# Performance work log

Measured on AMD Instinct MI355X. Metric: run time of the kernel, lower is better.

Reference implementation:

```python
import jax, jax.numpy as jnp
import numpy as np

SEQ, B = 128, 512
PT, EH, ZS, DH, NM, NMAX = 5, 256, 128, 512, 20, 256


def setup_inputs() -> dict:
    key = jax.random.key(0)
    ks = jax.random.split(key, 24)
    rn = lambda k, sh, sc=0.05: jax.random.normal(k, sh, dtype=jnp.float32) * sc
    return {
        "s": rn(ks[0], (SEQ, B, PT), 1.0),
        "enc_Wih_f": rn(ks[1], (4 * EH, PT)), "enc_Whh_f": rn(ks[2], (4 * EH, EH)), "enc_b_f": rn(ks[3], (4 * EH,)),
        "enc_Wih_b": rn(ks[4], (4 * EH, PT)), "enc_Whh_b": rn(ks[5], (4 * EH, EH)), "enc_b_b": rn(ks[6], (4 * EH,)),
        "Wmu": rn(ks[7], (ZS, 2 * EH)), "bmu": rn(ks[8], (ZS,)),
        "Wsig": rn(ks[9], (ZS, 2 * EH)), "bsig": rn(ks[10], (ZS,)),
        "Wh0": rn(ks[11], (DH, ZS)), "bh0": rn(ks[12], (DH,)),
        "dec_Wih": rn(ks[13], (4 * DH, PT + ZS)), "dec_Whh": rn(ks[14], (4 * DH, DH)), "dec_b": rn(ks[15], (4 * DH,)),
        "Wdec": rn(ks[16], (6 * NM + 3, DH)), "bdec": rn(ks[17], (6 * NM + 3,)),
        "z_eps": rn(ks[18], (B, ZS), 1.0),
        "gmm_eps": rn(ks[19], (NMAX, B, NM, 2), 1.0),
        "pen_u": jax.random.uniform(ks[20], (NMAX, B, 3), dtype=jnp.float32),
    }


def _lstm_dir(x, Wih, Whh, b, reverse):
    # PyTorch gate order: i, f, g, o. Returns final hidden state [B, H].
    H = Whh.shape[1]
    Bn = x.shape[1]
    def step(carry, xt):
        h, c = carry
        g = xt @ Wih.T + h @ Whh.T + b
        i, f, gg, o = jnp.split(g, 4, axis=-1)
        c = jax.nn.sigmoid(f) * c + jax.nn.sigmoid(i) * jnp.tanh(gg)
        h = jax.nn.sigmoid(o) * jnp.tanh(c)
        return (h, c), None
    init = (jnp.zeros((Bn, H), x.dtype), jnp.zeros((Bn, H), x.dtype))
    (h, _), _ = jax.lax.scan(step, init, x, reverse=reverse)
    return h


def reference(s, enc_Wih_f, enc_Whh_f, enc_b_f, enc_Wih_b, enc_Whh_b, enc_b_b,
              Wmu, bmu, Wsig, bsig, Wh0, bh0,
              dec_Wih, dec_Whh, dec_b, Wdec, bdec,
              z_eps, gmm_eps, pen_u):
    Bn = s.shape[1]
    # Bidirectional encoder -> concat last hidden states [B, 2*EH]
    hf = _lstm_dir(s, enc_Wih_f, enc_Whh_f, enc_b_f, False)
    hb = _lstm_dir(s, enc_Wih_b, enc_Whh_b, enc_b_b, True)
    h = jnp.concatenate([hf, hb], axis=-1)
    # Reparameterized latent
    mu = h @ Wmu.T + bmu
    sigma = jnp.exp((h @ Wsig.T + bsig) * 0.5)
    z = mu + sigma * z_eps                      # [B, ZS]
    h0 = jnp.tanh(z @ Wh0.T + bh0)              # [B, DH]
    c0 = jnp.zeros_like(h0)
    s0 = jnp.tile(jnp.array([0.0, 0.0, 1.0, 0.0, 0.0], jnp.float32), (Bn, 1))

    def step(carry, noise):
        prev, hc, cc = carry
        eps, u = noise                          # eps [B,NM,2], u [B,3]
        x = jnp.concatenate([prev, z], axis=-1)  # [B, PT+ZS]
        g = x @ dec_Wih.T + hc @ dec_Whh.T + dec_b
        i, f, gg, o = jnp.split(g, 4, axis=-1)
        cc = jax.nn.sigmoid(f) * cc + jax.nn.sigmoid(i) * jnp.tanh(gg)
        hc = jax.nn.sigmoid(o) * jnp.tanh(cc)
        y = hc @ Wdec.T + bdec                  # [B, 6*NM+3]
        mix = y[:, :6 * NM].reshape(Bn, NM, 6)
        pi = jax.nn.softmax(mix[..., 0], axis=-1)
        mx, my = mix[..., 1], mix[..., 2]
        sx, sy = jnp.exp(mix[..., 3]), jnp.exp(mix[..., 4])
        cor = jnp.tanh(mix[..., 5])
        # Sample from N(mean, [[sx^2, cor],[cor, sy^2]]) via Cholesky (cov as in source)
        l21 = cor / sx
        l22 = jnp.sqrt(jnp.maximum(sy * sy - l21 * l21, 1e-6))
        e1, e2 = eps[..., 0], eps[..., 1]
        samp_x = mx + sx * e1
        samp_y = my + l21 * e1 + l22 * e2
        dx = jnp.sum(pi * samp_x, axis=-1)      # pi-weighted sum over mixtures (as in source)
        dy = jnp.sum(pi * samp_y, axis=-1)
        q = jax.nn.softmax(y[:, -3:], axis=-1)
        pen = (u < q).astype(jnp.float32)       # independent Bernoulli thresholds, as in source
        point = jnp.concatenate([dx[:, None], dy[:, None], pen], axis=-1)
        return (point, hc, cc), point

    _, sketch = jax.lax.scan(step, (s0, h0, c0), (gmm_eps, pen_u))
    return sketch  # [NMAX, B, 5]
```

## Files before the change

### kernel.cpp

```cpp
#include <hip/hip_runtime.h>
#include <math.h>

#define B     512
#define SEQL  128
#define PT    5
#define EH    256
#define ZS    128
#define DH    512
#define NM    20
#define NMAXT 256

__device__ __forceinline__ float sigf(float x) { return 1.0f / (1.0f + expf(-x)); }

#define FMA8(m, av, lo, hi)                                                   \
    acc[m][0]=fmaf(av,lo.x,acc[m][0]); acc[m][1]=fmaf(av,lo.y,acc[m][1]);     \
    acc[m][2]=fmaf(av,lo.z,acc[m][2]); acc[m][3]=fmaf(av,lo.w,acc[m][3]);     \
    acc[m][4]=fmaf(av,hi.x,acc[m][4]); acc[m][5]=fmaf(av,hi.y,acc[m][5]);     \
    acc[m][6]=fmaf(av,hi.z,acc[m][6]); acc[m][7]=fmaf(av,hi.w,acc[m][7]);

#define XSUM(v) v += __shfl_xor(v,1); v += __shfl_xor(v,2); v += __shfl_xor(v,4); \
                v += __shfl_xor(v,8); v += __shfl_xor(v,16); v += __shfl_xor(v,32);

__global__ void transpose_pad(const float* __restrict__ in, float* __restrict__ out,
                              int rows, int cols, int rpad, long islice, long oslice)
{
    const float* ip = in + (size_t)blockIdx.z * islice;
    float* op = out + (size_t)blockIdx.z * oslice;
    int idx = blockIdx.x * 256 + threadIdx.x;
    if (idx >= cols * rpad) return;
    int c = idx / rpad, r = idx - c * rpad;
    op[idx] = (r < rows) ? ip[(size_t)r * cols + c] : 0.0f;
}

__global__ __launch_bounds__(256, 2) void enc_step3(
    const float* __restrict__ sT,
    const float* __restrict__ WihF, const float* __restrict__ WhhF, const float* __restrict__ bF,
    const float* __restrict__ WihB, const float* __restrict__ WhhB, const float* __restrict__ bB,
    const float* __restrict__ hfin, float* __restrict__ hfout, float* __restrict__ cf,
    const float* __restrict__ hbin, float* __restrict__ hbout, float* __restrict__ cb,
    int t)
{
    __shared__ float lds[8704];

    const int tid = threadIdx.x;
    const int x   = blockIdx.x;
    const int ng  = x & 31;
    const int bg  = (x >> 5) & 7;
    const int dir = x >> 8;
    const int n0  = ng * 8;
    const int b0  = bg * 64;

    const float* Whh  = dir ? WhhB : WhhF;
    const float* Wih  = dir ? WihB : WihF;
    const float* bias = dir ? bB   : bF;
    const float* hin  = dir ? hbin : hfin;
    float* hout       = dir ? hbout: hfout;
    float* c          = dir ? cb   : cf;
    const int ts = dir ? (SEQL - 1 - t) : t;

    #pragma unroll
    for (int i = 0; i < 8; ++i) {
        const int fidx = i * 256 + tid;
        const int w  = fidx >> 9;
        const int rem = fidx & 511;
        const int r  = rem >> 4, s5 = rem & 15;
        const int g  = r >> 3, nn = r & 7;
        const float4 wv = *(const float4*)&Whh[(size_t)(g * EH + n0 + nn) * EH + w * 64 + s5 * 4];
        *(float4*)&lds[((w * 32 + r) * 16 + (s5 ^ ((r >> 2) & 7))) * 4] = wv;
    }
    __syncthreads();

    const int lane = tid & 63;
    const int wv   = tid >> 6;
    const int ri   = lane & 7;
    const int bi   = lane >> 3;
    const float* hcol = hin + b0 + bi * 8;

    float acc[4][8];
    #pragma unroll
    for (int m = 0; m < 4; ++m)
        #pragma unroll
        for (int j = 0; j < 8; ++j) acc[m][j] = 0.0f;

    #pragma unroll 4
    for (int j4 = 0; j4 < 16; ++j4) {
        float4 a[4];
        #pragma unroll
        for (int m = 0; m < 4; ++m)
            a[m] = *(const float4*)&lds[((wv * 32 + ri * 4 + m) * 16 + (j4 ^ ri)) * 4];
        float4 blo[4], bhi[4];
        #pragma unroll
        for (int jj = 0; jj < 4; ++jj) {
            const float* hp = hcol + (size_t)(wv * 64 + j4 * 4 + jj) * B;
            blo[jj] = *(const float4*)hp;
            bhi[jj] = *(const float4*)(hp + 4);
        }
        #pragma unroll
        for (int m = 0; m < 4; ++m) {
            FMA8(m, a[m].x, blo[0], bhi[0])
            FMA8(m, a[m].y, blo[1], bhi[1])
            FMA8(m, a[m].z, blo[2], bhi[2])
            FMA8(m, a[m].w, blo[3], bhi[3])
        }
    }
    __syncthreads();

    #pragma unroll
    for (int m = 0; m < 4; ++m) {
        float* pr = &lds[(wv * 32 + ri * 4 + m) * 68 + bi * 8];
        *(float4*)pr       = make_float4(acc[m][0], acc[m][1], acc[m][2], acc[m][3]);
        *(float4*)(pr + 4) = make_float4(acc[m][4], acc[m][5], acc[m][6], acc[m][7]);
    }
    __syncthreads();

    const int nn = tid & 7;
    const int c0 = (tid >> 3) * 2;
    const int bgl = b0 + c0;

    float ps[4][2];
    #pragma unroll
    for (int g = 0; g < 4; ++g) {
        const int r = g * 8 + nn;
        ps[g][0] = lds[r * 68 + c0]     + lds[(32 + r) * 68 + c0]
                 + lds[(64 + r) * 68 + c0] + lds[(96 + r) * 68 + c0];
        ps[g][1] = lds[r * 68 + c0 + 1] + lds[(32 + r) * 68 + c0 + 1]
                 + lds[(64 + r) * 68 + c0 + 1] + lds[(96 + r) * 68 + c0 + 1];
    }

    #pragma unroll
    for (int bb2 = 0; bb2 < 2; ++bb2) {
        const int b = bgl + bb2;
        float gv[4];
        const float x0 = sT[((size_t)ts * PT + 0) * B + b];
        const float x1 = sT[((size_t)ts * PT + 1) * B + b];
        const float x2 = sT[((size_t)ts * PT + 2) * B + b];
        const float x3 = sT[((size_t)ts * PT + 3) * B + b];
        const float x4 = sT[((size_t)ts * PT + 4) * B + b];
        #pragma unroll
        for (int g = 0; g < 4; ++g) {
            const int grow = g * EH + n0 + nn;
            const float* wr = Wih + (size_t)grow * PT;
            float v = ps[g][bb2] + bias[grow];
            v = fmaf(x0, wr[0], v); v = fmaf(x1, wr[1], v); v = fmaf(x2, wr[2], v);
            v = fmaf(x3, wr[3], v); v = fmaf(x4, wr[4], v);
            gv[g] = v;
        }
        const size_t idx = (size_t)(n0 + nn) * B + b;
        const float cv = sigf(gv[1]) * c[idx] + sigf(gv[0]) * tanhf(gv[2]);
        c[idx] = cv;
        hout[idx] = sigf(gv[3]) * tanhf(cv);
    }
}

__global__ __launch_bounds__(256, 2) void dec_step3(
    const float* __restrict__ hin, float* __restrict__ hout, float* __restrict__ cT,
    const float* __restrict__ CzT, const float* __restrict__ Whh,
    const float* __restrict__ Wih, const float* __restrict__ prevPt, int t)
{
    __shared__ float lds[16384];

    const int tid = threadIdx.x;
    const int x   = blockIdx.x;
    const int ng  = x & 63;
    const int bg  = x >> 6;
    const int n0  = ng * 8;
    const int b0  = bg * 64;

    #pragma unroll
    for (int i = 0; i < 16; ++i) {
        const int fidx = i * 256 + tid;
        const int w   = fidx >> 10;
        const int rem = fidx & 1023;
        const int r   = rem >> 5, s5 = rem & 31;
        const int g   = r >> 3, nn = r & 7;
        const int sl  = (s5 & 16) | ((s5 & 15) ^ ((r >> 2) & 7));
        const float4 wv = *(const float4*)&Whh[(size_t)(g * DH + n0 + nn) * DH + w * 128 + s5 * 4];
        *(float4*)&lds[((w * 32 + r) * 32 + sl) * 4] = wv;
    }
    __syncthreads();

    const int lane = tid & 63;
    const int wv   = tid >> 6;
    const int ri   = lane & 7;
    const int bi   = lane >> 3;
    const float* hcol = hin + b0 + bi * 8;

    float acc[4][8];
    #pragma unroll
    for (int m = 0; m < 4; ++m)
        #pragma unroll
        for (int j = 0; j < 8; ++j) acc[m][j] = 0.0f;

    #pragma unroll
    for (int cc = 0; cc < 2; ++cc) {
        const int kb = wv * 128 + cc * 64;
        #pragma unroll 4
        for (int j4 = 0; j4 < 16; ++j4) {
            float4 a[4];
            #pragma unroll
            for (int m = 0; m < 4; ++m)
                a[m] = *(const float4*)&lds[((wv * 32 + ri * 4 + m) * 32 + cc * 16 + (j4 ^ ri)) * 4];
            float4 blo[4], bhi[4];
            #pragma unroll
            for (int jj = 0; jj < 4; ++jj) {
                const float* hp = hcol + (size_t)(kb + j4 * 4 + jj) * B;
                blo[jj] = *(const float4*)hp;
                bhi[jj] = *(const float4*)(hp + 4);
            }
            #pragma unroll
            for (int m = 0; m < 4; ++m) {
                FMA8(m, a[m].x, blo[0], bhi[0])
                FMA8(m, a[m].y, blo[1], bhi[1])
                FMA8(m, a[m].z, blo[2], bhi[2])
                FMA8(m, a[m].w, blo[3], bhi[3])
            }
        }
    }
    __syncthreads();

    #pragma unroll
    for (int m = 0; m < 4; ++m) {
        float* pr = &lds[(wv * 32 + ri * 4 + m) * 68 + bi * 8];
        *(float4*)pr       = make_float4(acc[m][0], acc[m][1], acc[m][2], acc[m][3]);
        *(float4*)(pr + 4) = make_float4(acc[m][4], acc[m][5], acc[m][6], acc[m][7]);
    }
    __syncthreads();

    const int nn = tid & 7;
    const int c0 = (tid >> 3) * 2;
    const int bgl = b0 + c0;

    float ps[4][2];
    #pragma unroll
    for (int g = 0; g < 4; ++g) {
        const int r = g * 8 + nn;
        ps[g][0] = lds[r * 68 + c0]     + lds[(32 + r) * 68 + c0]
                 + lds[(64 + r) * 68 + c0] + lds[(96 + r) * 68 + c0];
        ps[g][1] = lds[r * 68 + c0 + 1] + lds[(32 + r) * 68 + c0 + 1]
                 + lds[(64 + r) * 68 + c0 + 1] + lds[(96 + r) * 68 + c0 + 1];
    }

    #pragma unroll
    for (int bb2 = 0; bb2 < 2; ++bb2) {
        const int b = bgl + bb2;
        float p0, p1, p2, p3, p4;
        if (t == 0) { p0 = 0.f; p1 = 0.f; p2 = 1.f; p3 = 0.f; p4 = 0.f; }
        else {
            const float* pp = &prevPt[(size_t)b * 5];
            p0 = pp[0]; p1 = pp[1]; p2 = pp[2]; p3 = pp[3]; p4 = pp[4];
        }
        float gv[4];
        #pragma unroll
        for (int g = 0; g < 4; ++g) {
            const int grow = g * DH + n0 + nn;
            const float* wr = Wih + (size_t)grow * 133;
            float v = ps[g][bb2] + CzT[(size_t)grow * B + b];
            v = fmaf(p0, wr[0], v); v = fmaf(p1, wr[1], v); v = fmaf(p2, wr[2], v);
            v = fmaf(p3, wr[3], v); v = fmaf(p4, wr[4], v);
            gv[g] = v;
        }
        const size_t idx = (size_t)(n0 + nn) * B + b;
        const float cv = sigf(gv[1]) * cT[idx] + sigf(gv[0]) * tanhf(gv[2]);
        cT[idx] = cv;
        hout[idx] = sigf(gv[3]) * tanhf(cv);
    }
}

__global__ __launch_bounds__(256) void ysamp4(
    const float* __restrict__ hT, const float* __restrict__ WdecT,
    const float* __restrict__ bdec,
    const float* __restrict__ geps, const float* __restrict__ penu,
    float* __restrict__ out, int t)
{
    __shared__ float part[2][2][128];
    __shared__ float Y[2][128];

    const int tid = threadIdx.x;
    const int col = tid & 127;
    const int ks  = tid >> 7;
    const int b0  = blockIdx.x * 2;

    float a0 = 0.f, a1 = 0.f;
    const float* wp = WdecT + (size_t)ks * 256 * 128 + col;
    const float* hp = hT + (size_t)ks * 256 * B + b0;
    #pragma unroll 8
    for (int k = 0; k < 256; ++k) {
        const float w  = wp[(size_t)k * 128];
        const float2 h2 = *(const float2*)(hp + (size_t)k * B);
        a0 = fmaf(w, h2.x, a0);
        a1 = fmaf(w, h2.y, a1);
    }
    part[ks][0][col] = a0;
    part[ks][1][col] = a1;
    __syncthreads();
    if (ks == 0) {
        const float bd = (col < 123) ? bdec[col] : 0.0f;
        Y[0][col] = part[0][0][col] + part[1][0][col] + bd;
        Y[1][col] = part[0][1][col] + part[1][1][col] + bd;
    }
    __syncthreads();

    if (tid < 128) {
        const int bp   = tid >> 6;
        const int lane = tid & 63;
        const int b    = b0 + bp;
        const float* y = Y[bp];

        const int m = lane;
        float pv = (m < NM) ? y[6 * m] : -1e30f;
        float mm = pv;
        mm = fmaxf(mm, __shfl_xor(mm, 1));  mm = fmaxf(mm, __shfl_xor(mm, 2));
        mm = fmaxf(mm, __shfl_xor(mm, 4));  mm = fmaxf(mm, __shfl_xor(mm, 8));
        mm = fmaxf(mm, __shfl_xor(mm, 16)); mm = fmaxf(mm, __shfl_xor(mm, 32));
        float pe = 0.f, tx = 0.f, ty = 0.f;
        if (m < NM) {
            pe = expf(pv - mm);
            const float mx = y[6 * m + 1], my = y[6 * m + 2];
            const float sx = expf(y[6 * m + 3]), sy = expf(y[6 * m + 4]);
            const float cor = tanhf(y[6 * m + 5]);
            const float l21 = cor / sx;
            const float l22 = sqrtf(fmaxf(sy * sy - l21 * l21, 1e-6f));
            const float* ep = &geps[(((size_t)t * B) + b) * (NM * 2) + 2 * m];
            const float e1 = ep[0], e2 = ep[1];
            tx = pe * fmaf(sx, e1, mx);
            ty = pe * (my + fmaf(l21, e1, l22 * e2));
        }
        XSUM(pe) XSUM(tx) XSUM(ty)
        if (lane == 0) {
            const float q0 = y[120], q1 = y[121], q2 = y[122];
            const float qm = fmaxf(q0, fmaxf(q1, q2));
            const float e0 = expf(q0 - qm), e1q = expf(q1 - qm), e2q = expf(q2 - qm);
            const float qs = e0 + e1q + e2q;
            const float* u = &penu[(((size_t)t * B) + b) * 3];
            float* o = &out[(((size_t)t * B) + b) * 5];
            o[0] = tx / pe;
            o[1] = ty / pe;
            o[2] = (u[0] < e0  / qs) ? 1.f : 0.f;
            o[3] = (u[1] < e1q / qs) ? 1.f : 0.f;
            o[4] = (u[2] < e2q / qs) ? 1.f : 0.f;
        }
    }
}

__global__ __launch_bounds__(256) void latent2(
    const float* __restrict__ hfT, const float* __restrict__ hbT,
    const float* __restrict__ Wmu, const float* __restrict__ bmu,
    const float* __restrict__ Wsig, const float* __restrict__ bsig,
    const float* __restrict__ zepsT, float* __restrict__ zT)
{
    const int lane = threadIdx.x & 63;
    const int wv   = __builtin_amdgcn_readfirstlane(threadIdx.x >> 6);
    const int b    = blockIdx.x * 64 + lane;
    const int n0   = blockIdx.y * 8 + wv * 2;

    float am[2] = {}, as2[2] = {};
    #pragma unroll 4
    for (int k0 = 0; k0 < 2 * EH; k0 += 4) {
        const float* hsrc = (k0 < EH) ? hfT : hbT;
        const int kk = k0 & (EH - 1);
        const float a0 = hsrc[(size_t)(kk + 0) * B + b];
        const float a1 = hsrc[(size_t)(kk + 1) * B + b];
        const float a2 = hsrc[(size_t)(kk + 2) * B + b];
        const float a3 = hsrc[(size_t)(kk + 3) * B + b];
        #pragma unroll
        for (int j = 0; j < 2; ++j) {
            const float4 wm = *(const float4*)&Wmu[((size_t)(n0 + j)) * (2 * EH) + k0];
            const float4 ws = *(const float4*)&Wsig[((size_t)(n0 + j)) * (2 * EH) + k0];
            float u = am[j], v = as2[j];
            u = fmaf(a0, wm.x, u); u = fmaf(a1, wm.y, u); u = fmaf(a2, wm.z, u); u = fmaf(a3, wm.w, u);
            v = fmaf(a0, ws.x, v); v = fmaf(a1, ws.y, v); v = fmaf(a2, ws.z, v); v = fmaf(a3, ws.w, v);
            am[j] = u; as2[j] = v;
        }
    }
    #pragma unroll
    for (int j = 0; j < 2; ++j) {
        const int n = n0 + j;
        const float mu = am[j] + bmu[n];
        const float sg = expf(0.5f * (as2[j] + bsig[n]));
        zT[(size_t)n * B + b] = fmaf(sg, zepsT[(size_t)n * B + b], mu);
    }
}

__global__ __launch_bounds__(256) void h02(
    const float* __restrict__ zT, const float* __restrict__ Wh0,
    const float* __restrict__ bh0, float* __restrict__ hT)
{
    const int lane = threadIdx.x & 63;
    const int wv   = __builtin_amdgcn_readfirstlane(threadIdx.x >> 6);
    const int b    = blockIdx.x * 64 + lane;
    const int n0   = blockIdx.y * 32 + wv * 8;

    float acc[8] = {};
    #pragma unroll 2
    for (int k0 = 0; k0 < ZS; k0 += 4) {
        const float a0 = zT[(size_t)(k0 + 0) * B + b];
        const float a1 = zT[(size_t)(k0 + 1) * B + b];
        const float a2 = zT[(size_t)(k0 + 2) * B + b];
        const float a3 = zT[(size_t)(k0 + 3) * B + b];
        #pragma unroll
        for (int r = 0; r < 8; ++r) {
            const float4 w = *(const float4*)&Wh0[((size_t)(n0 + r)) * ZS + k0];
            float v = acc[r];
            v = fmaf(a0, w.x, v); v = fmaf(a1, w.y, v);
            v = fmaf(a2, w.z, v); v = fmaf(a3, w.w, v);
            acc[r] = v;
        }
    }
    #pragma unroll
    for (int r = 0; r < 8; ++r)
        hT[(size_t)(n0 + r) * B + b] = tanhf(acc[r] + bh0[n0 + r]);
}

__global__ __launch_bounds__(256) void cz2(
    const float* __restrict__ zT, const float* __restrict__ Wih,
    const float* __restrict__ bias, float* __restrict__ CzT)
{
    const int lane = threadIdx.x & 63;
    const int wv   = __builtin_amdgcn_readfirstlane(threadIdx.x >> 6);
    const int b    = blockIdx.x * 64 + lane;
    const int r0   = blockIdx.y * 32 + wv * 8;

    float acc[8] = {};
    #pragma unroll 4
    for (int k = 0; k < ZS; ++k) {
        const float a = zT[(size_t)k * B + b];
        #pragma unroll
        for (int r = 0; r < 8; ++r)
            acc[r] = fmaf(a, Wih[(size_t)(r0 + r) * 133 + 5 + k], acc[r]);
    }
    #pragma unroll
    for (int r = 0; r < 8; ++r)
        CzT[(size_t)(r0 + r) * B + b] = acc[r] + bias[r0 + r];
}

extern "C" void kernel_launch(void* const* d_in, const int* in_sizes, int n_in,
                              void* d_out, int out_size, void* d_ws, size_t ws_size,
                              hipStream_t stream)
{
    (void)in_sizes; (void)n_in; (void)out_size; (void)ws_size;

    const float* s      = (const float*)d_in[0];
    const float* WihF   = (const float*)d_in[1];
    const float* WhhF   = (const float*)d_in[2];
    const float* bF     = (const float*)d_in[3];
    const float* WihB   = (const float*)d_in[4];
    const float* WhhB   = (const float*)d_in[5];
    const float* bB     = (const float*)d_in[6];
    const float* Wmu    = (const float*)d_in[7];
    const float* bmu    = (const float*)d_in[8];
    const float* Wsig   = (const float*)d_in[9];
    const float* bsig   = (const float*)d_in[10];
    const float* Wh0    = (const float*)d_in[11];
    const float* bh0    = (const float*)d_in[12];
    const float* decWih = (const float*)d_in[13];
    const float* decWhh = (const float*)d_in[14];
    const float* decB   = (const float*)d_in[15];
    const float* Wdec   = (const float*)d_in[16];
    const float* bdec   = (const float*)d_in[17];
    const float* zeps   = (const float*)d_in[18];
    const float* geps   = (const float*)d_in[19];
    const float* penu   = (const float*)d_in[20];

    float* out = (float*)d_out;
    float* p   = (float*)d_ws;

    float* hf0  = p; p += 131072;
    float* hb0  = p; p += 131072;
    float* cf   = p; p += 131072;
    float* cb   = p; p += 131072;
    float* cdT  = p; p += 262144;
    float* hf1  = p; p += 131072;
    float* hb1  = p; p += 131072;
    float* hA   = p; p += 262144;
    float* hB   = p; p += 262144;
    float* zT   = p; p += 65536;
    float* CzT  = p; p += 1048576;
    float* zepsT= p; p += 65536;
    float* WdecT= p; p += 65536;
    float* sT   = p; p += 327680;

    hipMemsetAsync((void*)hf0, 0, (size_t)(4 * 131072 + 262144) * sizeof(float), stream);

    transpose_pad<<<dim3(256, 1, 1), 256, 0, stream>>>(zeps, zepsT, B, ZS, B, 0, 0);
    transpose_pad<<<dim3(256, 1, 1), 256, 0, stream>>>(Wdec, WdecT, 123, DH, 128, 0, 0);
    transpose_pad<<<dim3(10, 1, SEQL), 256, 0, stream>>>(s, sT, B, PT, B, (long)B * PT, (long)B * PT);

    for (int t = 0; t < SEQL; ++t) {
        const float* hfin = (t & 1) ? hf1 : hf0;  float* hfout = (t & 1) ? hf0 : hf1;
        const float* hbin = (t & 1) ? hb1 : hb0;  float* hbout = (t & 1) ? hb0 : hb1;
        enc_step3<<<dim3(512), 256, 0, stream>>>(
            sT, WihF, WhhF, bF, WihB, WhhB, bB,
            hfin, hfout, cf, hbin, hbout, cb, t);
    }
    latent2<<<dim3(8, 16), 256, 0, stream>>>(hf0, hb0, Wmu, bmu, Wsig, bsig, zepsT, zT);
    h02<<<dim3(8, 16), 256, 0, stream>>>(zT, Wh0, bh0, hA);
    cz2<<<dim3(8, 64), 256, 0, stream>>>(zT, decWih, decB, CzT);

    for (int t = 0; t < NMAXT; ++t) {
        const float* hin = (t & 1) ? hB : hA;
        float* hout      = (t & 1) ? hA : hB;
        dec_step3<<<dim3(512), 256, 0, stream>>>(
            hin, hout, cdT, CzT, decWhh, decWih,
            t ? (out + (size_t)(t - 1) * B * 5) : out, t);
        ysamp4<<<dim3(256), 256, 0, stream>>>(hout, WdecT, bdec, geps, penu, out, t);
    }
}
```

Baseline: 12.23 ms.

## Double threads per block and split K across 8 waves in LSTM step kernels

The encoder and decoder step kernels now launch with 512 threads, and the K reduction is split across 8 waves instead of 4, followed by an 8-way partial-sum reduction in LDS. Each thread's epilogue now handles one batch column instead of two. The output sampling kernel now uses one batch element per block with a 4-way K split over 512 blocks. The aim is more latency hiding and parallelism in these small, latency-bound recurrent steps, at the cost of larger LDS use and an extra reduction step.

```diff
diff --git a/kernel.cpp b/kernel.cpp
--- a/kernel.cpp
+++ b/kernel.cpp
@@ -32,7 +32,7 @@
     op[idx] = (r < rows) ? ip[(size_t)r * cols + c] : 0.0f;
 }
 
-__global__ __launch_bounds__(256, 2) void enc_step3(
+__global__ __launch_bounds__(512, 4) void enc_step4(
     const float* __restrict__ sT,
     const float* __restrict__ WihF, const float* __restrict__ WhhF, const float* __restrict__ bF,
     const float* __restrict__ WihB, const float* __restrict__ WhhB, const float* __restrict__ bB,
@@ -40,7 +40,7 @@
     const float* __restrict__ hbin, float* __restrict__ hbout, float* __restrict__ cb,
     int t)
 {
-    __shared__ float lds[8704];
+    __shared__ float lds[17408];
 
     const int tid = threadIdx.x;
     const int x   = blockIdx.x;
@@ -59,14 +59,14 @@
     const int ts = dir ? (SEQL - 1 - t) : t;
 
     #pragma unroll
-    for (int i = 0; i < 8; ++i) {
-        const int fidx = i * 256 + tid;
-        const int w  = fidx >> 9;
+    for (int i = 0; i < 4; ++i) {
+        const int fidx = i * 512 + tid;
+        const int w   = fidx >> 9;
         const int rem = fidx & 511;
-        const int r  = rem >> 4, s5 = rem & 15;
-        const int g  = r >> 3, nn = r & 7;
-        const float4 wv = *(const float4*)&Whh[(size_t)(g * EH + n0 + nn) * EH + w * 64 + s5 * 4];
-        *(float4*)&lds[((w * 32 + r) * 16 + (s5 ^ ((r >> 2) & 7))) * 4] = wv;
+        const int r   = rem >> 4, s5 = rem & 15;
+        const int g   = r >> 3, nn = r & 7;
+        const float4 wv4 = *(const float4*)&Whh[(size_t)(g * EH + n0 + nn) * EH + w * 64 + s5 * 4];
+        *(float4*)&lds[((w * 32 + r) * 16 + (s5 ^ ((r >> 2) & 7))) * 4] = wv4;
     }
     __syncthreads();
 
@@ -74,6 +74,8 @@
     const int wv   = tid >> 6;
     const int ri   = lane & 7;
     const int bi   = lane >> 3;
+    const int wq   = wv >> 1;
+    const int sb   = (wv & 1) * 8;
     const float* hcol = hin + b0 + bi * 8;
 
     float acc[4][8];
@@ -82,25 +84,23 @@
         #pragma unroll
         for (int j = 0; j < 8; ++j) acc[m][j] = 0.0f;
 
-    #pragma unroll 4
-    for (int j4 = 0; j4 < 16; ++j4) {
+    #pragma unroll 2
+    for (int j4 = 0; j4 < 8; ++j4) {
         float4 a[4];
         #pragma unroll
         for (int m = 0; m < 4; ++m)
-            a[m] = *(const float4*)&lds[((wv * 32 + ri * 4 + m) * 16 + (j4 ^ ri)) * 4];
-        float4 blo[4], bhi[4];
+            a[m] = *(const float4*)&lds[((wq * 32 + ri * 4 + m) * 16 + (sb | (j4 ^ ri))) * 4];
+        const int kb = wv * 32 + j4 * 4;
         #pragma unroll
         for (int jj = 0; jj < 4; ++jj) {
-            const float* hp = hcol + (size_t)(wv * 64 + j4 * 4 + jj) * B;
-            blo[jj] = *(const float4*)hp;
-            bhi[jj] = *(const float4*)(hp + 4);
-        }
-        #pragma unroll
-        for (int m = 0; m < 4; ++m) {
-            FMA8(m, a[m].x, blo[0], bhi[0])
-            FMA8(m, a[m].y, blo[1], bhi[1])
-            FMA8(m, a[m].z, blo[2], bhi[2])
-            FMA8(m, a[m].w, blo[3], bhi[3])
+            const float* hp = hcol + (size_t)(kb + jj) * B;
+            const float4 blo = *(const float4*)hp;
+            const float4 bhi = *(const float4*)(hp + 4);
+            #pragma unroll
+            for (int m = 0; m < 4; ++m) {
+                const float av = (jj == 0) ? a[m].x : (jj == 1) ? a[m].y : (jj == 2) ? a[m].z : a[m].w;
+                FMA8(m, av, blo, bhi)
+            }
         }
     }
     __syncthreads();
@@ -114,50 +114,46 @@
     __syncthreads();
 
     const int nn = tid & 7;
-    const int c0 = (tid >> 3) * 2;
-    const int bgl = b0 + c0;
-
-    float ps[4][2];
+    const int c0 = tid >> 3;
+    const int b  = b0 + c0;
+
+    float ps[4];
     #pragma unroll
     for (int g = 0; g < 4; ++g) {
         const int r = g * 8 + nn;
-        ps[g][0] = lds[r * 68 + c0]     + lds[(32 + r) * 68 + c0]
-                 + lds[(64 + r) * 68 + c0] + lds[(96 + r) * 68 + c0];
-        ps[g][1] = lds[r * 68 + c0 + 1] + lds[(32 + r) * 68 + c0 + 1]
-                 + lds[(64 + r) * 68 + c0 + 1] + lds[(96 + r) * 68 + c0 + 1];
-    }
-
-    #pragma unroll
-    for (int bb2 = 0; bb2 < 2; ++bb2) {
-        const int b = bgl + bb2;
-        float gv[4];
-        const float x0 = sT[((size_t)ts * PT + 0) * B + b];
-        const float x1 = sT[((size_t)ts * PT + 1) * B + b];
-        const float x2 = sT[((size_t)ts * PT + 2) * B + b];
-        const float x3 = sT[((size_t)ts * PT + 3) * B + b];
-        const float x4 = sT[((size_t)ts * PT + 4) * B + b];
-        #pragma unroll
-        for (int g = 0; g < 4; ++g) {
-            const int grow = g * EH + n0 + nn;
-            const float* wr = Wih + (size_t)grow * PT;
-            float v = ps[g][bb2] + bias[grow];
-            v = fmaf(x0, wr[0], v); v = fmaf(x1, wr[1], v); v = fmaf(x2, wr[2], v);
-            v = fmaf(x3, wr[3], v); v = fmaf(x4, wr[4], v);
-            gv[g] = v;
-        }
-        const size_t idx = (size_t)(n0 + nn) * B + b;
-        const float cv = sigf(gv[1]) * c[idx] + sigf(gv[0]) * tanhf(gv[2]);
-        c[idx] = cv;
-        hout[idx] = sigf(gv[3]) * tanhf(cv);
-    }
-}
-
-__global__ __launch_bounds__(256, 2) void dec_step3(
+        float v = 0.0f;
+        #pragma unroll
+        for (int w8 = 0; w8 < 8; ++w8) v += lds[(w8 * 32 + r) * 68 + c0];
+        ps[g] = v;
+    }
+
+    const float x0 = sT[((size_t)ts * PT + 0) * B + b];
+    const float x1 = sT[((size_t)ts * PT + 1) * B + b];
+    const float x2 = sT[((size_t)ts * PT + 2) * B + b];
+    const float x3 = sT[((size_t)ts * PT + 3) * B + b];
+    const float x4 = sT[((size_t)ts * PT + 4) * B + b];
+    float gv[4];
+    #pragma unroll
+    for (int g = 0; g < 4; ++g) {
+        const int grow = g * EH + n0 + nn;
+        const float* wr = Wih + (size_t)grow * PT;
+        float v = ps[g] + bias[grow];
+        v = fmaf(x0, wr[0], v); v = fmaf(x1, wr[1], v); v = fmaf(x2, wr[2], v);
+        v = fmaf(x3, wr[3], v); v = fmaf(x4, wr[4], v);
+        gv[g] = v;
+    }
+    const size_t idx = (size_t)(n0 + nn) * B + b;
+    const float cv = sigf(gv[1]) * c[idx] + sigf(gv[0]) * tanhf(gv[2]);
+    c[idx] = cv;
+    hout[idx] = sigf(gv[3]) * tanhf(cv);
+}
+
+__global__ __launch_bounds__(512, 4) void dec_step4(
     const float* __restrict__ hin, float* __restrict__ hout, float* __restrict__ cT,
     const float* __restrict__ CzT, const float* __restrict__ Whh,
     const float* __restrict__ Wih, const float* __restrict__ prevPt, int t)
 {
-    __shared__ float lds[16384];
+    __shared__ float lds[17408];
 
     const int tid = threadIdx.x;
     const int x   = blockIdx.x;
@@ -167,15 +163,15 @@
     const int b0  = bg * 64;
 
     #pragma unroll
-    for (int i = 0; i < 16; ++i) {
-        const int fidx = i * 256 + tid;
+    for (int i = 0; i < 8; ++i) {
+        const int fidx = i * 512 + tid;
         const int w   = fidx >> 10;
         const int rem = fidx & 1023;
         const int r   = rem >> 5, s5 = rem & 31;
         const int g   = r >> 3, nn = r & 7;
         const int sl  = (s5 & 16) | ((s5 & 15) ^ ((r >> 2) & 7));
-        const float4 wv = *(const float4*)&Whh[(size_t)(g * DH + n0 + nn) * DH + w * 128 + s5 * 4];
-        *(float4*)&lds[((w * 32 + r) * 32 + sl) * 4] = wv;
+        const float4 wv4 = *(const float4*)&Whh[(size_t)(g * DH + n0 + nn) * DH + w * 128 + s5 * 4];
+        *(float4*)&lds[((w * 32 + r) * 32 + sl) * 4] = wv4;
     }
     __syncthreads();
 
@@ -183,6 +179,8 @@
     const int wv   = tid >> 6;
     const int ri   = lane & 7;
     const int bi   = lane >> 3;
+    const int wq   = wv >> 1;
+    const int sb   = (wv & 1) * 16;
     const float* hcol = hin + b0 + bi * 8;
 
     float acc[4][8];
@@ -191,28 +189,22 @@
         #pragma unroll
         for (int j = 0; j < 8; ++j) acc[m][j] = 0.0f;
 
-    #pragma unroll
-    for (int cc = 0; cc < 2; ++cc) {
-        const int kb = wv * 128 + cc * 64;
-        #pragma unroll 4
-        for (int j4 = 0; j4 < 16; ++j4) {
-            float4 a[4];
-            #pragma unroll
-            for (int m = 0; m < 4; ++m)
-                a[m] = *(const float4*)&lds[((wv * 32 + ri * 4 + m) * 32 + cc * 16 + (j4 ^ ri)) * 4];
-            float4 blo[4], bhi[4];
-            #pragma unroll
-            for (int jj = 0; jj < 4; ++jj) {
-                const float* hp = hcol + (size_t)(kb + j4 * 4 + jj) * B;
-                blo[jj] = *(const float4*)hp;
-                bhi[jj] = *(const float4*)(hp + 4);
-            }
+    #pragma unroll 2
+    for (int j4 = 0; j4 < 16; ++j4) {
+        float4 a[4];
+        #pragma unroll
+        for (int m = 0; m < 4; ++m)
+            a[m] = *(const float4*)&lds[((wq * 32 + ri * 4 + m) * 32 + (sb | (j4 ^ ri))) * 4];
+        const int kb = wv * 64 + j4 * 4;
+        #pragma unroll
+        for (int jj = 0; jj < 4; ++jj) {
+            const float* hp = hcol + (size_t)(kb + jj) * B;
+            const float4 blo = *(const float4*)hp;
+            const float4 bhi = *(const float4*)(hp + 4);
             #pragma unroll
             for (int m = 0; m < 4; ++m) {
-                FMA8(m, a[m].x, blo[0], bhi[0])
-                FMA8(m, a[m].y, blo[1], bhi[1])
-                FMA8(m, a[m].z, blo[2], bhi[2])
-                FMA8(m, a[m].w, blo[3], bhi[3])
+                const float av = (jj == 0) ? a[m].x : (jj == 1) ? a[m].y : (jj == 2) ? a[m].z : a[m].w;
+                FMA8(m, av, blo, bhi)
             }
         }
     }
@@ -227,85 +219,71 @@
     __syncthreads();
 
     const int nn = tid & 7;
-    const int c0 = (tid >> 3) * 2;
-    const int bgl = b0 + c0;
-
-    float ps[4][2];
+    const int c0 = tid >> 3;
+    const int b  = b0 + c0;
+
+    float ps[4];
     #pragma unroll
     for (int g = 0; g < 4; ++g) {
         const int r = g * 8 + nn;
-        ps[g][0] = lds[r * 68 + c0]     + lds[(32 + r) * 68 + c0]
-                 + lds[(64 + r) * 68 + c0] + lds[(96 + r) * 68 + c0];
-        ps[g][1] = lds[r * 68 + c0 + 1] + lds[(32 + r) * 68 + c0 + 1]
-                 + lds[(64 + r) * 68 + c0 + 1] + lds[(96 + r) * 68 + c0 + 1];
-    }
-
-    #pragma unroll
-    for (int bb2 = 0; bb2 < 2; ++bb2) {
-        const int b = bgl + bb2;
-        float p0, p1, p2, p3, p4;
-        if (t == 0) { p0 = 0.f; p1 = 0.f; p2 = 1.f; p3 = 0.f; p4 = 0.f; }
-        else {
-            const float* pp = &prevPt[(size_t)b * 5];
-            p0 = pp[0]; p1 = pp[1]; p2 = pp[2]; p3 = pp[3]; p4 = pp[4];
-        }
-        float gv[4];
-        #pragma unroll
-        for (int g = 0; g < 4; ++g) {
-            const int grow = g * DH + n0 + nn;
-            const float* wr = Wih + (size_t)grow * 133;
-            float v = ps[g][bb2] + CzT[(size_t)grow * B + b];
-            v = fmaf(p0, wr[0], v); v = fmaf(p1, wr[1], v); v = fmaf(p2, wr[2], v);
-            v = fmaf(p3, wr[3], v); v = fmaf(p4, wr[4], v);
-            gv[g] = v;
-        }
-        const size_t idx = (size_t)(n0 + nn) * B + b;
-        const float cv = sigf(gv[1]) * cT[idx] + sigf(gv[0]) * tanhf(gv[2]);
-        cT[idx] = cv;
-        hout[idx] = sigf(gv[3]) * tanhf(cv);
-    }
-}
-
-__global__ __launch_bounds__(256) void ysamp4(
+        float v = 0.0f;
+        #pragma unroll
+        for (int w8 = 0; w8 < 8; ++w8) v += lds[(w8 * 32 + r) * 68 + c0];
+        ps[g] = v;
+    }
+
+    float p0, p1, p2, p3, p4;
+    if (t == 0) { p0 = 0.f; p1 = 0.f; p2 = 1.f; p3 = 0.f; p4 = 0.f; }
+    else {
+        const float* pp = &prevPt[(size_t)b * 5];
+        p0 = pp[0]; p1 = pp[1]; p2 = pp[2]; p3 = pp[3]; p4 = pp[4];
+    }
+    float gv[4];
+    #pragma unroll
+    for (int g = 0; g < 4; ++g) {
+        const int grow = g * DH + n0 + nn;
+        const float* wr = Wih + (size_t)grow * 133;
+        float v = ps[g] + CzT[(size_t)grow * B + b];
+        v = fmaf(p0, wr[0], v); v = fmaf(p1, wr[1], v); v = fmaf(p2, wr[2], v);
+        v = fmaf(p3, wr[3], v); v = fmaf(p4, wr[4], v);
+        gv[g] = v;
+    }
+    const size_t idx = (size_t)(n0 + nn) * B + b;
+    const float cv = sigf(gv[1]) * cT[idx] + sigf(gv[0]) * tanhf(gv[2]);
+    cT[idx] = cv;
+    hout[idx] = sigf(gv[3]) * tanhf(cv);
+}
+
+__global__ __launch_bounds__(512) void ysamp5(
     const float* __restrict__ hT, const float* __restrict__ WdecT,
     const float* __restrict__ bdec,
     const float* __restrict__ geps, const float* __restrict__ penu,
     float* __restrict__ out, int t)
 {
-    __shared__ float part[2][2][128];
-    __shared__ float Y[2][128];
+    __shared__ float part[4][128];
+    __shared__ float Y[128];
 
     const int tid = threadIdx.x;
     const int col = tid & 127;
     const int ks  = tid >> 7;
-    const int b0  = blockIdx.x * 2;
-
-    float a0 = 0.f, a1 = 0.f;
-    const float* wp = WdecT + (size_t)ks * 256 * 128 + col;
-    const float* hp = hT + (size_t)ks * 256 * B + b0;
+    const int b   = blockIdx.x;
+
+    float a0 = 0.f;
+    const float* wp = WdecT + (size_t)ks * 128 * 128 + col;
+    const float* hp = hT + (size_t)ks * 128 * B + b;
     #pragma unroll 8
-    for (int k = 0; k < 256; ++k) {
-        const float w  = wp[(size_t)k * 128];
-        const float2 h2 = *(const float2*)(hp + (size_t)k * B);
-        a0 = fmaf(w, h2.x, a0);
-        a1 = fmaf(w, h2.y, a1);
-    }
-    part[ks][0][col] = a0;
-    part[ks][1][col] = a1;
-    __syncthreads();
-    if (ks == 0) {
-        const float bd = (col < 123) ? bdec[col] : 0.0f;
-        Y[0][col] = part[0][0][col] + part[1][0][col] + bd;
-        Y[1][col] = part[0][1][col] + part[1][1][col] + bd;
-    }
-    __syncthreads();
-
-    if (tid < 128) {
-        const int bp   = tid >> 6;
-        const int lane = tid & 63;
-        const int b    = b0 + bp;
-        const float* y = Y[bp];
-
+    for (int k = 0; k < 128; ++k)
+        a0 = fmaf(wp[(size_t)k * 128], hp[(size_t)k * B], a0);
+    part[ks][col] = a0;
+    __syncthreads();
+    if (ks == 0)
+        Y[col] = part[0][col] + part[1][col] + part[2][col] + part[3][col]
+               + ((col < 123) ? bdec[col] : 0.0f);
+    __syncthreads();
+
+    if (tid < 64) {
+        const int lane = tid;
+        const float* y = Y;
         const int m = lane;
         float pv = (m < NM) ? y[6 * m] : -1e30f;
         float mm = pv;
@@ -488,7 +466,7 @@
     for (int t = 0; t < SEQL; ++t) {
         const float* hfin = (t & 1) ? hf1 : hf0;  float* hfout = (t & 1) ? hf0 : hf1;
         const float* hbin = (t & 1) ? hb1 : hb0;  float* hbout = (t & 1) ? hb0 : hb1;
-        enc_step3<<<dim3(512), 256, 0, stream>>>(
+        enc_step4<<<dim3(512), 512, 0, stream>>>(
             sT, WihF, WhhF, bF, WihB, WhhB, bB,
             hfin, hfout, cf, hbin, hbout, cb, t);
     }
@@ -499,9 +477,9 @@
     for (int t = 0; t < NMAXT; ++t) {
         const float* hin = (t & 1) ? hB : hA;
         float* hout      = (t & 1) ? hA : hB;
-        dec_step3<<<dim3(512), 256, 0, stream>>>(
+        dec_step4<<<dim3(512), 512, 0, stream>>>(
             hin, hout, cdT, CzT, decWhh, decWih,
             t ? (out + (size_t)(t - 1) * B * 5) : out, t);
-        ysamp4<<<dim3(256), 256, 0, stream>>>(hout, WdecT, bdec, geps, penu, out, t);
-    }
-}
+        ysamp5<<<dim3(512), 512, 0, stream>>>(hout, WdecT, bdec, geps, penu, out, t);
+    }
+}
```

Measured after the change: 11.07 ms. 9.5% less time.
